# Performance work log

Hardware: AMD Instinct MI355X
Metric: run time of the kernel (lower is better)

Reference implementation:

```python
import jax, jax.numpy as jnp
import numpy as np

RATIO = 0.25
RADIUS = 0.2
K = 32  # PyG radius() default max_num_neighbors


def fps(pos, n_samples):
    """Farthest point sampling for one cloud. pos: [N,3] -> indices [S]."""
    d2 = jnp.sum((pos - pos[0]) ** 2, axis=-1)  # dist to first (deterministic start)
    idx0 = jnp.zeros((n_samples,), jnp.int32)

    def body(i, state):
        idx, d = state
        nxt = jnp.argmax(d).astype(jnp.int32)
        idx = idx.at[i].set(nxt)
        d = jnp.minimum(d, jnp.sum((pos - pos[nxt]) ** 2, axis=-1))
        return idx, d

    idx, _ = jax.lax.fori_loop(1, n_samples, body, (idx0, d2))
    return idx


def setup_inputs() -> dict:
    key = jax.random.key(0)
    k0, k1, k2, k3 = jax.random.split(key, 4)
    B, N, C = 16, 4096, 64
    x = jax.random.normal(k0, (B, N, C), jnp.float32)
    pos = jax.random.uniform(k1, (B, N, 3), jnp.float32)  # unit cube
    W1 = jax.random.normal(k2, (C + 3, 128), jnp.float32) / np.sqrt(C + 3).astype(np.float32)
    b1 = jnp.zeros((128,), jnp.float32)
    W2 = jax.random.normal(k3, (128, 256), jnp.float32) / np.sqrt(128).astype(np.float32)
    b2 = jnp.zeros((256,), jnp.float32)
    return {"x": x, "pos": pos, "W1": W1, "b1": b1, "W2": W2, "b2": b2}


def reference(x, pos, W1, b1, W2, b2):
    B, N, C = x.shape
    S = int(N * RATIO)
    r2 = RADIUS * RADIUS

    # --- FPS per cloud ---
    samp = jax.vmap(lambda p: fps(p, S))(pos)            # [B,S] int32
    pos_s = jnp.take_along_axis(pos, samp[..., None], axis=1)  # [B,S,3]

    # --- ball query: K nearest within radius of each centroid ---
    d2 = jnp.sum((pos_s[:, :, None, :] - pos[:, None, :, :]) ** 2, axis=-1)  # [B,S,N]
    neg = jnp.where(d2 <= r2, -d2, -jnp.inf)
    negk, nbr = jax.lax.top_k(neg, K)                    # [B,S,K]
    valid = negk > -jnp.inf                              # centroid itself (d2=0) always valid

    # --- gather -> local MLP -> max pool (PointConv with max aggregation) ---
    x_j = jax.vmap(lambda xb, nb: xb[nb])(x, nbr)        # [B,S,K,C]
    pos_j = jax.vmap(lambda pb, nb: pb[nb])(pos, nbr)    # [B,S,K,3]
    rel = pos_j - pos_s[:, :, None, :]                   # pos_j - pos_i
    h = jnp.concatenate([x_j, rel], axis=-1)             # [B,S,K,C+3]
    h = jax.nn.relu(jnp.einsum("bskc,cd->bskd", h, W1) + b1)
    h = jax.nn.relu(jnp.einsum("bskd,de->bske", h, W2) + b2)
    h = jnp.where(valid[..., None], h, -jnp.inf)
    out = jnp.max(h, axis=2)                             # [B,S,256]
    return out, pos_s
```

## Files before the change

kernel.cpp:

```cpp
#include <hip/hip_runtime.h>
#include <stdint.h>

typedef unsigned short u16;
typedef unsigned int u32;
typedef unsigned long long u64;

#define NB 16
#define NP 4096
#define NCH 64
#define NS 1024
#define NK 32
#define H1D 128
#define H2D 256
#define KP1 96
#define LDA 104
#define LDH 136
#define OUTOFF (NB * NS * H2D)

typedef __attribute__((ext_vector_type(8))) short bfrag;
typedef __attribute__((ext_vector_type(4))) float facc4;
typedef __attribute__((ext_vector_type(2))) float f32x2;

__device__ __forceinline__ u16 f2bf(float f) {
  u32 u = __float_as_uint(f);
  u += 0x7FFFu + ((u >> 16) & 1u);
  return (u16)(u >> 16);
}

__device__ __forceinline__ float dist2(float ax, float ay, float az,
                                       float bx, float by, float bz) {
#pragma clang fp contract(off)
  float dx = ax - bx, dy = ay - by, dz = az - bz;
  return dx * dx + dy * dy + dz * dz;
}

__device__ __forceinline__ f32x2 dist2v(f32x2 ax, f32x2 ay, f32x2 az,
                                        float bx, float by, float bz) {
#pragma clang fp contract(off)
  f32x2 dx = ax - bx, dy = ay - by, dz = az - bz;
  return dx * dx + dy * dy + dz * dz;
}

__device__ __forceinline__ float wave_max_f32(float v) {
  const int NI = (int)0xFF800000u;
  v = fmaxf(v, __int_as_float(__builtin_amdgcn_update_dpp(NI, __float_as_int(v), 0x111, 0xf, 0xf, false)));
  v = fmaxf(v, __int_as_float(__builtin_amdgcn_update_dpp(NI, __float_as_int(v), 0x112, 0xf, 0xf, false)));
  v = fmaxf(v, __int_as_float(__builtin_amdgcn_update_dpp(NI, __float_as_int(v), 0x114, 0xf, 0xf, false)));
  v = fmaxf(v, __int_as_float(__builtin_amdgcn_update_dpp(NI, __float_as_int(v), 0x118, 0xf, 0xf, false)));
  v = fmaxf(v, __int_as_float(__builtin_amdgcn_update_dpp(NI, __float_as_int(v), 0x142, 0xa, 0xf, false)));
  v = fmaxf(v, __int_as_float(__builtin_amdgcn_update_dpp(NI, __float_as_int(v), 0x143, 0xc, 0xf, false)));
  return __int_as_float(__builtin_amdgcn_readlane(__float_as_int(v), 63));
}

__device__ __forceinline__ u32 wave_min_u32(u32 v) {
  u32 t;
  t = (u32)__builtin_amdgcn_update_dpp(-1, (int)v, 0x111, 0xf, 0xf, false); v = t < v ? t : v;
  t = (u32)__builtin_amdgcn_update_dpp(-1, (int)v, 0x112, 0xf, 0xf, false); v = t < v ? t : v;
  t = (u32)__builtin_amdgcn_update_dpp(-1, (int)v, 0x114, 0xf, 0xf, false); v = t < v ? t : v;
  t = (u32)__builtin_amdgcn_update_dpp(-1, (int)v, 0x118, 0xf, 0xf, false); v = t < v ? t : v;
  t = (u32)__builtin_amdgcn_update_dpp(-1, (int)v, 0x142, 0xa, 0xf, false); v = t < v ? t : v;
  t = (u32)__builtin_amdgcn_update_dpp(-1, (int)v, 0x143, 0xc, 0xf, false); v = t < v ? t : v;
  return (u32)__builtin_amdgcn_readlane((int)v, 63);
}

#define QUAD_MAX_STEP(CTRL)                                                           \
  {                                                                                   \
    const u32 plo = (u32)__builtin_amdgcn_update_dpp(0, (int)klo, (CTRL), 0xf, 0xf, true); \
    const u32 phi = (u32)__builtin_amdgcn_update_dpp(0, (int)khi, (CTRL), 0xf, 0xf, true); \
    const u32 pqx = (u32)__builtin_amdgcn_update_dpp(0, (int)qxu, (CTRL), 0xf, 0xf, true); \
    const u32 pqy = (u32)__builtin_amdgcn_update_dpp(0, (int)qyu, (CTRL), 0xf, 0xf, true); \
    const u32 pqz = (u32)__builtin_amdgcn_update_dpp(0, (int)qzu, (CTRL), 0xf, 0xf, true); \
    const u64 ok = ((u64)phi << 32) | plo;                                            \
    const u64 mk = ((u64)khi << 32) | klo;                                            \
    if (ok > mk) { klo = plo; khi = phi; qxu = pqx; qyu = pqy; qzu = pqz; }           \
  }

__global__ void setup_kernel(const float* __restrict__ W1, const float* __restrict__ W2,
                             u16* __restrict__ W1T, u16* __restrict__ W2T) {
  int idx = blockIdx.x * 256 + threadIdx.x;
  if (idx < H1D * KP1) {
    int n = idx / KP1, k = idx % KP1;
    W1T[idx] = f2bf(k < 67 ? W1[k * H1D + n] : 0.f);
  } else if (idx < H1D * KP1 + H2D * H1D) {
    int j = idx - H1D * KP1;
    int n = j / H1D, k = j % H1D;
    W2T[j] = f2bf(W2[k * H2D + n]);
  }
}

__global__ __launch_bounds__(256) void fps_kernel(const float* __restrict__ pos,
                                                  int* __restrict__ samp,
                                                  float* __restrict__ pos_s) {
  __shared__ float4 plds[NP];
  __shared__ __align__(16) u32 recs[2][4][8];
  __shared__ u16 gilist[NS];
  const int b = blockIdx.x;
  const int tid = threadIdx.x;
  const int lane = tid & 63, wv = tid >> 6;
  const float* pb = pos + (size_t)b * NP * 3;
  for (int k = tid; k < NP; k += 256)
    plds[k] = make_float4(pb[k * 3 + 0], pb[k * 3 + 1], pb[k * 3 + 2], 0.f);
  if (tid == 0) gilist[0] = 0;
  __syncthreads();

  f32x2 px2[8], py2[8], pz2[8], dd[8];
  const float4 q0 = plds[0];
  float bv = -1.f;
  int bj = 0;
#pragma unroll
  for (int t = 0; t < 8; ++t) {
    const float4 pA = plds[tid * 16 + 2 * t];
    const float4 pB = plds[tid * 16 + 2 * t + 1];
    px2[t] = (f32x2){pA.x, pB.x};
    py2[t] = (f32x2){pA.y, pB.y};
    pz2[t] = (f32x2){pA.z, pB.z};
    const f32x2 s = dist2v(px2[t], py2[t], pz2[t], q0.x, q0.y, q0.z);
    dd[t] = s;
    const bool c0 = s.x > bv; bv = c0 ? s.x : bv; bj = c0 ? 2 * t : bj;
    const bool c1 = s.y > bv; bv = c1 ? s.y : bv; bj = c1 ? 2 * t + 1 : bj;
  }

  for (int i = 1; i < NS; ++i) {
    const int gidx = tid * 16 + bj;
    const float4 cpos = plds[gidx];
    const float wmax = wave_max_f32(bv);
    const u64 mask = __ballot(bv == wmax);
    const bool winner = (bv == wmax) && ((mask & ((1ull << lane) - 1ull)) == 0ull);
    if (winner) {
      u32* rp = &recs[i & 1][wv][0];
      *(uint4*)rp = make_uint4(4095u - (u32)gidx, __float_as_uint(bv),
                               __float_as_uint(cpos.x), __float_as_uint(cpos.y));
      rp[4] = __float_as_uint(cpos.z);
    }
    __syncthreads();
    const u32* sp = &recs[i & 1][lane & 3][0];
    const uint4 rA = *(const uint4*)sp;
    u32 klo = rA.x, khi = rA.y, qxu = rA.z, qyu = rA.w, qzu = sp[4];
    QUAD_MAX_STEP(0xB1)
    QUAD_MAX_STEP(0x4E)
    const float qx = __uint_as_float(qxu);
    const float qy = __uint_as_float(qyu);
    const float qz = __uint_as_float(qzu);
    if (tid == 0) gilist[i] = (u16)(4095 - (int)(klo & 0xFFFu));
    bv = -1.f; bj = 0;
#pragma unroll
    for (int t = 0; t < 8; ++t) {
      const f32x2 s = dist2v(px2[t], py2[t], pz2[t], qx, qy, qz);
      dd[t].x = fminf(dd[t].x, s.x);
      dd[t].y = fminf(dd[t].y, s.y);
      const bool c0 = dd[t].x > bv; bv = c0 ? dd[t].x : bv; bj = c0 ? 2 * t : bj;
      const bool c1 = dd[t].y > bv; bv = c1 ? dd[t].y : bv; bj = c1 ? 2 * t + 1 : bj;
    }
  }
  __syncthreads();
  for (int k = tid; k < NS; k += 256) {
    const int gi = (int)gilist[k];
    const float4 q = plds[gi];
    samp[b * NS + k] = gi;
    pos_s[((size_t)b * NS + k) * 3 + 0] = q.x;
    pos_s[((size_t)b * NS + k) * 3 + 1] = q.y;
    pos_s[((size_t)b * NS + k) * 3 + 2] = q.z;
  }
}

__global__ __launch_bounds__(256) void ballq_kernel(const float* __restrict__ pos,
                                                    const int* __restrict__ samp,
                                                    int* __restrict__ nbr) {
  __shared__ u64 buf[4][256];
  const int lane = threadIdx.x & 63, wv = threadIdx.x >> 6;
  const int sg = blockIdx.x * 4 + wv;
  const int b = sg >> 10;
  const int nc = samp[sg];
  const float* pb = pos + (size_t)b * NP * 3;
  const float cx = pb[nc * 3 + 0], cy = pb[nc * 3 + 1], cz = pb[nc * 3 + 2];
  const float r2 = (float)(0.2 * 0.2);
  int V = 0;
  for (int c = 0; c < 64; ++c) {
    const int i = c * 64 + lane;
    const float d2v = dist2(cx, cy, cz, pb[i * 3 + 0], pb[i * 3 + 1], pb[i * 3 + 2]);
    const bool valid = d2v <= r2;
    const u64 bal = __ballot(valid);
    if (valid) {
      const int rank = __popcll(bal & ((1ull << lane) - 1ull));
      const int p = V + rank;
      if (p < 256) buf[wv][p] = ((u64)__float_as_uint(d2v) << 32) | (u32)i;
    }
    V += __popcll(bal);
  }
  if (V > 256) V = 256;
  u32 kd[4], ki[4];
#pragma unroll
  for (int t = 0; t < 4; ++t) {
    const int p = t * 64 + lane;
    const u64 v = (p < V) ? buf[wv][p] : ~0ull;
    kd[t] = (u32)(v >> 32);
    ki[t] = (u32)v;
  }
  u32 my = 0, pad = 0;
  for (int e = 0; e < 32; ++e) {
    u32 m0 = kd[0] < kd[1] ? kd[0] : kd[1];
    u32 m1 = kd[2] < kd[3] ? kd[2] : kd[3];
    const u32 m = wave_min_u32(m0 < m1 ? m0 : m1);
    u32 ci = 0xFFFFFFFFu;
#pragma unroll
    for (int t = 0; t < 4; ++t) {
      const u32 cm = (ki[t] < ci) ? ki[t] : ci;
      ci = (kd[t] == m) ? cm : ci;
    }
    const u32 wi = wave_min_u32(ci);
    if (e == 0) pad = wi;
    const u32 sel = (m == 0xFFFFFFFFu) ? pad : wi;
    if (lane == e) my = sel;
#pragma unroll
    for (int t = 0; t < 4; ++t)
      if (ki[t] == wi) kd[t] = 0xFFFFFFFFu;
  }
  if (lane < 32) nbr[(size_t)sg * NK + lane] = (int)my;
}

__global__ __launch_bounds__(256) void mlp_kernel(
    const float* __restrict__ x, const float* __restrict__ pos,
    const float* __restrict__ b1, const float* __restrict__ b2,
    const int* __restrict__ nbr, const u16* __restrict__ W1T,
    const u16* __restrict__ W2T, const float* __restrict__ pos_s,
    float* __restrict__ out) {
  __shared__ u16 A[128 * LDA];
  __shared__ u16 Hs[128 * LDH];
  const int ctr0 = blockIdx.x * 4;
  const int b = ctr0 >> 10;
  const int tid = threadIdx.x;
  {
    const int row = tid >> 1, half = tid & 1;
    const int g = ctr0 + (row >> 5);
    const int n = nbr[(size_t)g * NK + (row & 31)];
    const float4* xr = (const float4*)(x + ((size_t)b * NP + n) * NCH + half * 32);
#pragma unroll
    for (int qq = 0; qq < 4; ++qq) {
      const float4 v0 = xr[2 * qq], v1 = xr[2 * qq + 1];
      uint4 wp;
      wp.x = (u32)f2bf(v0.x) | ((u32)f2bf(v0.y) << 16);
      wp.y = (u32)f2bf(v0.z) | ((u32)f2bf(v0.w) << 16);
      wp.z = (u32)f2bf(v1.x) | ((u32)f2bf(v1.y) << 16);
      wp.w = (u32)f2bf(v1.z) | ((u32)f2bf(v1.w) << 16);
      *(uint4*)&A[row * LDA + half * 32 + qq * 8] = wp;
    }
    if (half == 0) {
      const float rx = pos[((size_t)b * NP + n) * 3 + 0] - pos_s[(size_t)g * 3 + 0];
      const float ry = pos[((size_t)b * NP + n) * 3 + 1] - pos_s[(size_t)g * 3 + 1];
      const float rz = pos[((size_t)b * NP + n) * 3 + 2] - pos_s[(size_t)g * 3 + 2];
      uint4 wr;
      wr.x = (u32)f2bf(rx) | ((u32)f2bf(ry) << 16);
      wr.y = (u32)f2bf(rz);
      wr.z = 0; wr.w = 0;
      uint4 wz;
      wz.x = wz.y = wz.z = wz.w = 0;
      *(uint4*)&A[row * LDA + 64] = wr;
      *(uint4*)&A[row * LDA + 72] = wz;
      *(uint4*)&A[row * LDA + 80] = wz;
      *(uint4*)&A[row * LDA + 88] = wz;
    }
  }
  __syncthreads();
  const int lane = tid & 63, w = tid >> 6;
  const int r16 = lane & 15, g4 = lane >> 4;
  {
    bfrag af[2][3];
#pragma unroll
    for (int mg2 = 0; mg2 < 2; ++mg2)
#pragma unroll
      for (int ks = 0; ks < 3; ++ks)
        af[mg2][ks] = *(const bfrag*)&A[((2 * w + mg2) * 16 + r16) * LDA + ks * 32 + g4 * 8];
#pragma unroll
    for (int ng = 0; ng < 8; ++ng) {
      const bfrag bw0 = *(const bfrag*)&W1T[(ng * 16 + r16) * KP1 + 0 + g4 * 8];
      const bfrag bw1 = *(const bfrag*)&W1T[(ng * 16 + r16) * KP1 + 32 + g4 * 8];
      const bfrag bw2 = *(const bfrag*)&W1T[(ng * 16 + r16) * KP1 + 64 + g4 * 8];
      facc4 a0 = {0.f, 0.f, 0.f, 0.f}, a1 = {0.f, 0.f, 0.f, 0.f};
      a0 = __builtin_amdgcn_mfma_f32_16x16x32_bf16(bw0, af[0][0], a0, 0, 0, 0);
      a0 = __builtin_amdgcn_mfma_f32_16x16x32_bf16(bw1, af[0][1], a0, 0, 0, 0);
      a0 = __builtin_amdgcn_mfma_f32_16x16x32_bf16(bw2, af[0][2], a0, 0, 0, 0);
      a1 = __builtin_amdgcn_mfma_f32_16x16x32_bf16(bw0, af[1][0], a1, 0, 0, 0);
      a1 = __builtin_amdgcn_mfma_f32_16x16x32_bf16(bw1, af[1][1], a1, 0, 0, 0);
      a1 = __builtin_amdgcn_mfma_f32_16x16x32_bf16(bw2, af[1][2], a1, 0, 0, 0);
      const float4 bias4 = *(const float4*)&b1[ng * 16 + g4 * 4];
      const int nb = ng * 16 + g4 * 4;
      u32 lo0 = (u32)f2bf(fmaxf(a0[0] + bias4.x, 0.f)) | ((u32)f2bf(fmaxf(a0[1] + bias4.y, 0.f)) << 16);
      u32 hi0 = (u32)f2bf(fmaxf(a0[2] + bias4.z, 0.f)) | ((u32)f2bf(fmaxf(a0[3] + bias4.w, 0.f)) << 16);
      u32 lo1 = (u32)f2bf(fmaxf(a1[0] + bias4.x, 0.f)) | ((u32)f2bf(fmaxf(a1[1] + bias4.y, 0.f)) << 16);
      u32 hi1 = (u32)f2bf(fmaxf(a1[2] + bias4.z, 0.f)) | ((u32)f2bf(fmaxf(a1[3] + bias4.w, 0.f)) << 16);
      *(uint2*)&Hs[((2 * w + 0) * 16 + r16) * LDH + nb] = make_uint2(lo0, hi0);
      *(uint2*)&Hs[((2 * w + 1) * 16 + r16) * LDH + nb] = make_uint2(lo1, hi1);
    }
  }
  __syncthreads();
  {
    bfrag hf[2][4];
#pragma unroll
    for (int mg2 = 0; mg2 < 2; ++mg2)
#pragma unroll
      for (int ks = 0; ks < 4; ++ks)
        hf[mg2][ks] = *(const bfrag*)&Hs[((2 * w + mg2) * 16 + r16) * LDH + ks * 32 + g4 * 8];
    const int gout = ctr0 + w;
    const int NI = (int)0xFF800000u;
#pragma unroll
    for (int ng = 0; ng < 16; ++ng) {
      facc4 a0 = {0.f, 0.f, 0.f, 0.f}, a1 = {0.f, 0.f, 0.f, 0.f};
#pragma unroll
      for (int ks = 0; ks < 4; ++ks) {
        const bfrag bw = *(const bfrag*)&W2T[(ng * 16 + r16) * H1D + ks * 32 + g4 * 8];
        a0 = __builtin_amdgcn_mfma_f32_16x16x32_bf16(bw, hf[0][ks], a0, 0, 0, 0);
        a1 = __builtin_amdgcn_mfma_f32_16x16x32_bf16(bw, hf[1][ks], a1, 0, 0, 0);
      }
      float v0 = fmaxf(a0[0], a1[0]);
      float v1 = fmaxf(a0[1], a1[1]);
      float v2 = fmaxf(a0[2], a1[2]);
      float v3 = fmaxf(a0[3], a1[3]);
      v0 = fmaxf(v0, __int_as_float(__builtin_amdgcn_update_dpp(NI, __float_as_int(v0), 0x111, 0xf, 0xf, false)));
      v1 = fmaxf(v1, __int_as_float(__builtin_amdgcn_update_dpp(NI, __float_as_int(v1), 0x111, 0xf, 0xf, false)));
      v2 = fmaxf(v2, __int_as_float(__builtin_amdgcn_update_dpp(NI, __float_as_int(v2), 0x111, 0xf, 0xf, false)));
      v3 = fmaxf(v3, __int_as_float(__builtin_amdgcn_update_dpp(NI, __float_as_int(v3), 0x111, 0xf, 0xf, false)));
      v0 = fmaxf(v0, __int_as_float(__builtin_amdgcn_update_dpp(NI, __float_as_int(v0), 0x112, 0xf, 0xf, false)));
      v1 = fmaxf(v1, __int_as_float(__builtin_amdgcn_update_dpp(NI, __float_as_int(v1), 0x112, 0xf, 0xf, false)));
      v2 = fmaxf(v2, __int_as_float(__builtin_amdgcn_update_dpp(NI, __float_as_int(v2), 0x112, 0xf, 0xf, false)));
      v3 = fmaxf(v3, __int_as_float(__builtin_amdgcn_update_dpp(NI, __float_as_int(v3), 0x112, 0xf, 0xf, false)));
      v0 = fmaxf(v0, __int_as_float(__builtin_amdgcn_update_dpp(NI, __float_as_int(v0), 0x114, 0xf, 0xf, false)));
      v1 = fmaxf(v1, __int_as_float(__builtin_amdgcn_update_dpp(NI, __float_as_int(v1), 0x114, 0xf, 0xf, false)));
      v2 = fmaxf(v2, __int_as_float(__builtin_amdgcn_update_dpp(NI, __float_as_int(v2), 0x114, 0xf, 0xf, false)));
      v3 = fmaxf(v3, __int_as_float(__builtin_amdgcn_update_dpp(NI, __float_as_int(v3), 0x114, 0xf, 0xf, false)));
      v0 = fmaxf(v0, __int_as_float(__builtin_amdgcn_update_dpp(NI, __float_as_int(v0), 0x118, 0xf, 0xf, false)));
      v1 = fmaxf(v1, __int_as_float(__builtin_amdgcn_update_dpp(NI, __float_as_int(v1), 0x118, 0xf, 0xf, false)));
      v2 = fmaxf(v2, __int_as_float(__builtin_amdgcn_update_dpp(NI, __float_as_int(v2), 0x118, 0xf, 0xf, false)));
      v3 = fmaxf(v3, __int_as_float(__builtin_amdgcn_update_dpp(NI, __float_as_int(v3), 0x118, 0xf, 0xf, false)));
      if ((lane & 15) == 15) {
        const float4 b24 = *(const float4*)&b2[ng * 16 + g4 * 4];
        float4 o;
        o.x = fmaxf(v0 + b24.x, 0.f);
        o.y = fmaxf(v1 + b24.y, 0.f);
        o.z = fmaxf(v2 + b24.z, 0.f);
        o.w = fmaxf(v3 + b24.w, 0.f);
        *(float4*)&out[(size_t)gout * H2D + ng * 16 + g4 * 4] = o;
      }
    }
  }
}

extern "C" void kernel_launch(void* const* d_in, const int* in_sizes, int n_in,
                              void* d_out, int out_size, void* d_ws, size_t ws_size,
                              hipStream_t stream) {
  const float* x = (const float*)d_in[0];
  const float* pos = (const float*)d_in[1];
  const float* W1 = (const float*)d_in[2];
  const float* b1 = (const float*)d_in[3];
  const float* W2 = (const float*)d_in[4];
  const float* b2 = (const float*)d_in[5];
  float* out = (float*)d_out;
  char* ws = (char*)d_ws;
  u16* W1T = (u16*)(ws + 0);
  u16* W2T = (u16*)(ws + 24576);
  int* samp = (int*)(ws + 90112);
  int* nbr = (int*)(ws + 155648);
  float* pos_s = out + OUTOFF;

  setup_kernel<<<dim3(176), dim3(256), 0, stream>>>(W1, W2, W1T, W2T);
  fps_kernel<<<dim3(NB), dim3(256), 0, stream>>>(pos, samp, pos_s);
  ballq_kernel<<<dim3(NB * NS / 4), dim3(256), 0, stream>>>(pos, samp, nbr);
  mlp_kernel<<<dim3(NB * NS / 4), dim3(256), 0, stream>>>(x, pos, b1, b2, nbr, W1T, W2T,
                                                          pos_s, out);
}
```

Before: 919.4 us.

## Fuse ball query into MLP kernel and vectorize FPS argmax

Merges the ball-query kernel into the MLP kernel. Each wave finds the 32 neighbours of its centroid and writes them to shared memory, which the gather stage then reads; the ball-query buffer shares LDS with the A tile. This removes one launch and the global round trip for the neighbour indices. Separately, the FPS per-thread argmax is changed from a serial compare-select chain to a max tree followed by an equality bitmask and ctz, which shortens the dependency chain inside the serial FPS loop. The fused kernel uses more shared memory (~62KB), which may lower occupancy for the MLP phase.

```diff
diff --git a/kernel.cpp b/kernel.cpp
--- a/kernel.cpp
+++ b/kernel.cpp
@@ -142,15 +142,26 @@
     const float qy = __uint_as_float(qyu);
     const float qz = __uint_as_float(qzu);
     if (tid == 0) gilist[i] = (u16)(4095 - (int)(klo & 0xFFFu));
-    bv = -1.f; bj = 0;
 #pragma unroll
     for (int t = 0; t < 8; ++t) {
       const f32x2 s = dist2v(px2[t], py2[t], pz2[t], qx, qy, qz);
       dd[t].x = fminf(dd[t].x, s.x);
       dd[t].y = fminf(dd[t].y, s.y);
-      const bool c0 = dd[t].x > bv; bv = c0 ? dd[t].x : bv; bj = c0 ? 2 * t : bj;
-      const bool c1 = dd[t].y > bv; bv = c1 ? dd[t].y : bv; bj = c1 ? 2 * t + 1 : bj;
-    }
+    }
+    float v8[8];
+#pragma unroll
+    for (int t = 0; t < 8; ++t) v8[t] = fmaxf(dd[t].x, dd[t].y);
+    const float m0 = fmaxf(fmaxf(v8[0], v8[1]), fmaxf(v8[2], v8[3]));
+    const float m1 = fmaxf(fmaxf(v8[4], v8[5]), fmaxf(v8[6], v8[7]));
+    bv = fmaxf(m0, m1);
+    u32 e8[8];
+#pragma unroll
+    for (int t = 0; t < 8; ++t)
+      e8[t] = ((dd[t].x == bv) ? (1u << (2 * t)) : 0u) |
+              ((dd[t].y == bv) ? (1u << (2 * t + 1)) : 0u);
+    const u32 msk = (e8[0] | e8[1]) | (e8[2] | e8[3]) |
+                    ((e8[4] | e8[5]) | (e8[6] | e8[7]));
+    bj = (int)__builtin_ctz(msk);
   }
   __syncthreads();
   for (int k = tid; k < NS; k += 256) {
@@ -163,76 +174,77 @@
   }
 }
 
-__global__ __launch_bounds__(256) void ballq_kernel(const float* __restrict__ pos,
-                                                    const int* __restrict__ samp,
-                                                    int* __restrict__ nbr) {
-  __shared__ u64 buf[4][256];
-  const int lane = threadIdx.x & 63, wv = threadIdx.x >> 6;
-  const int sg = blockIdx.x * 4 + wv;
-  const int b = sg >> 10;
-  const int nc = samp[sg];
-  const float* pb = pos + (size_t)b * NP * 3;
-  const float cx = pb[nc * 3 + 0], cy = pb[nc * 3 + 1], cz = pb[nc * 3 + 2];
-  const float r2 = (float)(0.2 * 0.2);
-  int V = 0;
-  for (int c = 0; c < 64; ++c) {
-    const int i = c * 64 + lane;
-    const float d2v = dist2(cx, cy, cz, pb[i * 3 + 0], pb[i * 3 + 1], pb[i * 3 + 2]);
-    const bool valid = d2v <= r2;
-    const u64 bal = __ballot(valid);
-    if (valid) {
-      const int rank = __popcll(bal & ((1ull << lane) - 1ull));
-      const int p = V + rank;
-      if (p < 256) buf[wv][p] = ((u64)__float_as_uint(d2v) << 32) | (u32)i;
-    }
-    V += __popcll(bal);
-  }
-  if (V > 256) V = 256;
-  u32 kd[4], ki[4];
-#pragma unroll
-  for (int t = 0; t < 4; ++t) {
-    const int p = t * 64 + lane;
-    const u64 v = (p < V) ? buf[wv][p] : ~0ull;
-    kd[t] = (u32)(v >> 32);
-    ki[t] = (u32)v;
-  }
-  u32 my = 0, pad = 0;
-  for (int e = 0; e < 32; ++e) {
-    u32 m0 = kd[0] < kd[1] ? kd[0] : kd[1];
-    u32 m1 = kd[2] < kd[3] ? kd[2] : kd[3];
-    const u32 m = wave_min_u32(m0 < m1 ? m0 : m1);
-    u32 ci = 0xFFFFFFFFu;
-#pragma unroll
-    for (int t = 0; t < 4; ++t) {
-      const u32 cm = (ki[t] < ci) ? ki[t] : ci;
-      ci = (kd[t] == m) ? cm : ci;
-    }
-    const u32 wi = wave_min_u32(ci);
-    if (e == 0) pad = wi;
-    const u32 sel = (m == 0xFFFFFFFFu) ? pad : wi;
-    if (lane == e) my = sel;
-#pragma unroll
-    for (int t = 0; t < 4; ++t)
-      if (ki[t] == wi) kd[t] = 0xFFFFFFFFu;
-  }
-  if (lane < 32) nbr[(size_t)sg * NK + lane] = (int)my;
-}
-
-__global__ __launch_bounds__(256) void mlp_kernel(
+__global__ __launch_bounds__(256) void tail_kernel(
     const float* __restrict__ x, const float* __restrict__ pos,
     const float* __restrict__ b1, const float* __restrict__ b2,
-    const int* __restrict__ nbr, const u16* __restrict__ W1T,
+    const int* __restrict__ samp, const u16* __restrict__ W1T,
     const u16* __restrict__ W2T, const float* __restrict__ pos_s,
     float* __restrict__ out) {
-  __shared__ u16 A[128 * LDA];
-  __shared__ u16 Hs[128 * LDH];
+  __shared__ __align__(16) unsigned char smem[61968];
+  u64* qbuf = (u64*)smem;
+  u16* A = (u16*)smem;
+  u16* Hs = (u16*)(smem + 26624);
+  int* s_nbr = (int*)(smem + 61440);
+  int* s_nc = (int*)(smem + 61952);
+  const int tid = threadIdx.x;
+  const int lane = tid & 63, w = tid >> 6;
   const int ctr0 = blockIdx.x * 4;
   const int b = ctr0 >> 10;
-  const int tid = threadIdx.x;
+  const float* pb = pos + (size_t)b * NP * 3;
+  {
+    const int nc = samp[ctr0 + w];
+    const float cx = pb[nc * 3 + 0], cy = pb[nc * 3 + 1], cz = pb[nc * 3 + 2];
+    const float r2 = (float)(0.2 * 0.2);
+    u64* qb = qbuf + (size_t)w * 256;
+    int V = 0;
+    for (int c = 0; c < 64; ++c) {
+      const int i = c * 64 + lane;
+      const float d2v = dist2(cx, cy, cz, pb[i * 3 + 0], pb[i * 3 + 1], pb[i * 3 + 2]);
+      const bool valid = d2v <= r2;
+      const u64 bal = __ballot(valid);
+      if (valid) {
+        const int rank = __popcll(bal & ((1ull << lane) - 1ull));
+        const int p = V + rank;
+        if (p < 256) qb[p] = ((u64)__float_as_uint(d2v) << 32) | (u32)i;
+      }
+      V += __popcll(bal);
+    }
+    if (V > 256) V = 256;
+    u32 kd[4], ki[4];
+#pragma unroll
+    for (int t = 0; t < 4; ++t) {
+      const int p = t * 64 + lane;
+      const u64 v = (p < V) ? qb[p] : ~0ull;
+      kd[t] = (u32)(v >> 32);
+      ki[t] = (u32)v;
+    }
+    u32 my = 0, pad = 0;
+    for (int e = 0; e < 32; ++e) {
+      u32 m0 = kd[0] < kd[1] ? kd[0] : kd[1];
+      u32 m1 = kd[2] < kd[3] ? kd[2] : kd[3];
+      const u32 m = wave_min_u32(m0 < m1 ? m0 : m1);
+      u32 ci = 0xFFFFFFFFu;
+#pragma unroll
+      for (int t = 0; t < 4; ++t) {
+        const u32 cm = (ki[t] < ci) ? ki[t] : ci;
+        ci = (kd[t] == m) ? cm : ci;
+      }
+      const u32 wi = wave_min_u32(ci);
+      if (e == 0) pad = wi;
+      const u32 sel = (m == 0xFFFFFFFFu) ? pad : wi;
+      if (lane == e) my = sel;
+#pragma unroll
+      for (int t = 0; t < 4; ++t)
+        if (ki[t] == wi) kd[t] = 0xFFFFFFFFu;
+    }
+    if (lane < 32) s_nbr[w * 32 + lane] = (int)my;
+    if (lane == 0) s_nc[w] = nc;
+  }
+  __syncthreads();
   {
     const int row = tid >> 1, half = tid & 1;
     const int g = ctr0 + (row >> 5);
-    const int n = nbr[(size_t)g * NK + (row & 31)];
+    const int n = s_nbr[(row >> 5) * 32 + (row & 31)];
     const float4* xr = (const float4*)(x + ((size_t)b * NP + n) * NCH + half * 32);
 #pragma unroll
     for (int qq = 0; qq < 4; ++qq) {
@@ -261,7 +273,6 @@
     }
   }
   __syncthreads();
-  const int lane = tid & 63, w = tid >> 6;
   const int r16 = lane & 15, g4 = lane >> 4;
   {
     bfrag af[2][3];
@@ -358,12 +369,10 @@
   u16* W1T = (u16*)(ws + 0);
   u16* W2T = (u16*)(ws + 24576);
   int* samp = (int*)(ws + 90112);
-  int* nbr = (int*)(ws + 155648);
   float* pos_s = out + OUTOFF;
 
   setup_kernel<<<dim3(176), dim3(256), 0, stream>>>(W1, W2, W1T, W2T);
   fps_kernel<<<dim3(NB), dim3(256), 0, stream>>>(pos, samp, pos_s);
-  ballq_kernel<<<dim3(NB * NS / 4), dim3(256), 0, stream>>>(pos, samp, nbr);
-  mlp_kernel<<<dim3(NB * NS / 4), dim3(256), 0, stream>>>(x, pos, b1, b2, nbr, W1T, W2T,
-                                                          pos_s, out);
-}
+  tail_kernel<<<dim3(NB * NS / 4), dim3(256), 0, stream>>>(x, pos, b1, b2, samp, W1T,
+                                                           W2T, pos_s, out);
+}
```

Result: slower. 1.029 ms (+11.9%).
